# Kernel optimization log

Hardware: AMD Instinct MI355X
Metric: run time of the kernel (lower is better)

## Reference

```python
import jax, jax.numpy as jnp
import numpy as np

NUM_REGIONS = 20
EMBED_DIM = 768
PATCH = (4, 16, 16)          # (pd, ph, pw)
IMG = (64, 512, 512)         # (D, H, W)
B = 2
N_PATCHES = 16384


def setup_inputs() -> dict:
    key = jax.random.key(0)
    k1, k2, k3 = jax.random.split(key, 3)
    segmentation_mask = jax.random.randint(
        k1, (B, 1) + IMG, 0, NUM_REGIONS + 1, dtype=jnp.int32)
    patch_coords = jax.random.uniform(k2, (B, N_PATCHES, 3), dtype=jnp.float32)
    region_prototypes = 0.02 * jax.random.normal(
        k3, (NUM_REGIONS, EMBED_DIM), dtype=jnp.float32)
    return {"segmentation_mask": segmentation_mask,
            "patch_coords": patch_coords,
            "region_prototypes": region_prototypes}


def _compute_assignments(segmentation_mask, patch_coords):
    Bsz, _, D, H, W = segmentation_mask.shape
    pd, ph, pw = PATCH
    dims = jnp.array([D, H, W], dtype=jnp.float32)
    half = jnp.array([pd // 2, ph // 2, pw // 2], dtype=jnp.float32)

    cpix = patch_coords * dims                                   # (B,N,3)
    # torch: z_start = max(0, int(c - half)); z_end = min(D, int(c + half))
    start = jnp.maximum(0.0, jnp.floor(cpix - half)).astype(jnp.int32)   # (B,N,3)
    end = jnp.minimum(dims, jnp.floor(cpix + half)).astype(jnp.int32)    # (B,N,3)

    # per-axis index grids of fixed size, validity mask honors clipped box
    zi = start[..., 0:1] + jnp.arange(pd, dtype=jnp.int32)        # (B,N,pd)
    yi = start[..., 1:2] + jnp.arange(ph, dtype=jnp.int32)        # (B,N,ph)
    xi = start[..., 2:3] + jnp.arange(pw, dtype=jnp.int32)        # (B,N,pw)
    vz = zi < end[..., 0:1]
    vy = yi < end[..., 1:2]
    vx = xi < end[..., 2:3]

    ziC = jnp.clip(zi, 0, D - 1)
    yiC = jnp.clip(yi, 0, H - 1)
    xiC = jnp.clip(xi, 0, W - 1)

    # flattened gather: (B, N, pd, ph, pw) voxel values
    lin = (ziC[:, :, :, None, None] * (H * W)
           + yiC[:, :, None, :, None] * W
           + xiC[:, :, None, None, :])
    flat = segmentation_mask.reshape(Bsz, D * H * W)
    vals = jnp.take_along_axis(flat, lin.reshape(Bsz, -1), axis=1)
    vals = vals.reshape(Bsz, lin.shape[1], pd, ph, pw)
    valid = (vz[:, :, :, None, None]
             & vy[:, :, None, :, None]
             & vx[:, :, None, None, :])

    # numel of each (possibly clipped) crop
    extents = jnp.maximum(end - start, 0)                         # (B,N,3)
    numel = jnp.prod(extents, axis=-1).astype(jnp.float32)        # (B,N)

    # per-region counts; small fixed loop over 20 regions keeps memory low
    counts = jnp.stack(
        [jnp.sum((vals == r) & valid, axis=(2, 3, 4)).astype(jnp.float32)
         for r in range(1, NUM_REGIONS + 1)], axis=-1)            # (B,N,R)

    prop = counts / jnp.maximum(numel, 1.0)[..., None]            # zero crops -> 0
    a = prop + 1e-6
    a = a / jnp.sum(a, axis=-1, keepdims=True)
    return a


def reference(segmentation_mask, patch_coords, region_prototypes):
    Bsz = segmentation_mask.shape[0]
    region_features = jnp.broadcast_to(
        region_prototypes[None], (Bsz,) + region_prototypes.shape)
    patch_to_region = _compute_assignments(segmentation_mask, patch_coords)
    return region_features, patch_to_region
```

## Files before the change

kernel.cpp:

```cpp
#include <hip/hip_runtime.h>
#include <stdint.h>

#define NREG   20
#define EDIM   768
#define DVOL   64
#define HVOL   512
#define WVOL   512
#define HW_    (HVOL * WVOL)
#define DHW_   (DVOL * HVOL * WVOL)
#define NPATCH 16384
#define BTOT   2
#define PROTO_N (NREG * EDIM)
#define RF_N    (BTOT * PROTO_N)
#define TOTAL_PATCHES (BTOT * NPATCH)
#define NBUCKET 1024
#define SORT_BLOCKS 8

#define W_PHASE 0
#define W_BCNT  32
#define W_PID   (W_BCNT + SORT_BLOCKS * NBUCKET)
#define W_C0    (W_PID  + TOTAL_PATCHES)
#define W_C1    (W_C0   + TOTAL_PATCHES)
#define W_C2    (W_C1   + TOTAL_PATCHES)
#define MEMSET_WORDS (W_BCNT + SORT_BLOCKS * NBUCKET)

struct __attribute__((packed, aligned(4))) int4p { int x, y, z, w; };

__global__ __launch_bounds__(1024) void sort_kernel(
    const float* __restrict__ coords, unsigned* __restrict__ ws)
{
    __shared__ unsigned lcnt[NBUCKET];
    __shared__ unsigned lofs[NBUCKET];

    float* wsf = (float*)ws;
    const int blk = (int)blockIdx.x;
    const int t   = (int)threadIdx.x;
    const int p0  = blk * 4096 + t * 4;
    const int b   = blk >> 2;

    lcnt[t] = 0u;
    __syncthreads();

    float c[12];
    {
        const float4* cp = (const float4*)(coords + (size_t)p0 * 3);
        const float4 a = cp[0], bb = cp[1], d = cp[2];
        c[0]=a.x;  c[1]=a.y;  c[2]=a.z;  c[3]=a.w;  c[4]=bb.x; c[5]=bb.y;
        c[6]=bb.z; c[7]=bb.w; c[8]=d.x;  c[9]=d.y;  c[10]=d.z; c[11]=d.w;
    }
    unsigned key[4];
#pragma unroll
    for (int i = 0; i < 4; ++i) {
        const int zbin = ((int)(c[3*i + 0] * 64.0f))  >> 1;
        const int ybin = ((int)(c[3*i + 1] * 512.0f)) >> 5;
        key[i] = (unsigned)(b * 512 + zbin * 16 + ybin);
        atomicAdd(&lcnt[key[i]], 1u);
    }
    __syncthreads();

    ws[W_BCNT + blk * NBUCKET + t] = lcnt[t];
    __syncthreads();

    if (t == 0) {
        __hip_atomic_fetch_add(&ws[W_PHASE], 1u,
                               __ATOMIC_RELEASE, __HIP_MEMORY_SCOPE_AGENT);
        int guard = 0;
        while (__hip_atomic_load(&ws[W_PHASE],
                 __ATOMIC_ACQUIRE, __HIP_MEMORY_SCOPE_AGENT) < SORT_BLOCKS
               && guard < (1 << 22)) {
            __builtin_amdgcn_s_sleep(1);
            ++guard;
        }
    }
    __syncthreads();

    unsigned tot = 0u, before = 0u;
#pragma unroll
    for (int k = 0; k < SORT_BLOCKS; ++k) {
        const unsigned v = ws[W_BCNT + k * NBUCKET + t];
        tot += v;
        before += (k < blk) ? v : 0u;
    }
    lcnt[t] = tot;
    __syncthreads();

#pragma unroll
    for (int off = 1; off < NBUCKET; off <<= 1) {
        const unsigned u = (t >= off) ? lcnt[t - off] : 0u;
        __syncthreads();
        lcnt[t] += u;
        __syncthreads();
    }
    lofs[t] = (lcnt[t] - tot) + before;
    __syncthreads();

#pragma unroll
    for (int i = 0; i < 4; ++i) {
        const unsigned rank = atomicAdd(&lofs[key[i]], 1u);
        ws[W_PID + rank] = (unsigned)(p0 + i);
        wsf[W_C0 + rank] = c[3*i + 0];
        wsf[W_C1 + rank] = c[3*i + 1];
        wsf[W_C2 + rank] = c[3*i + 2];
    }
}

__global__ __launch_bounds__(256) void assign_kernel(
    const int*      __restrict__ seg,
    const unsigned* __restrict__ ws,
    const float*    __restrict__ proto,
    float*          __restrict__ out)
{
    if (blockIdx.x < RF_N / 256) {
        const int i = (int)blockIdx.x * 256 + (int)threadIdx.x;
        out[i] = proto[i >= PROTO_N ? i - PROTO_N : i];
    }

    const int bid  = (int)blockIdx.x;
    const int sbid = (bid & 7) * 1024 + (bid >> 3);

    const int lane = threadIdx.x & 63;
    const int wave = threadIdx.x >> 6;
    const int slot = sbid * 4 + wave;

    const int   patch = (int)ws[W_PID + slot];
    const float c0 = ((const float*)ws)[W_C0 + slot] * 64.0f;
    const float c1 = ((const float*)ws)[W_C1 + slot] * 512.0f;
    const float c2 = ((const float*)ws)[W_C2 + slot] * 512.0f;
    const int b = patch >> 14;

    const int sz = (int)fmaxf(0.0f,   floorf(c0 - 2.0f));
    const int ez = (int)fminf(64.0f,  floorf(c0 + 2.0f));
    const int sy = (int)fmaxf(0.0f,   floorf(c1 - 8.0f));
    const int ey = (int)fminf(512.0f, floorf(c1 + 8.0f));
    const int sx = (int)fmaxf(0.0f,   floorf(c2 - 8.0f));
    const int ex = (int)fminf(512.0f, floorf(c2 + 8.0f));

    const int xl4  = lane & 3;
    const int yy   = lane >> 2;
    const int p_lo = sx + 4 * xl4;
    const int st   = min(p_lo, WVOL - 4);
    const int yi   = sy + yy;
    const unsigned vy = (yi < ey) ? 0xFFFFFFFFu : 0u;
    const int yiC  = min(yi, HVOL - 1);
    const int rowbase = b * DHW_ + yiC * WVOL + st;

    unsigned vm[4];
#pragma unroll
    for (int j = 0; j < 4; ++j) {
        const int pos = st + j;
        vm[j] = (pos >= p_lo && pos < ex) ? vy : 0u;
    }

    int4p q0, q1, q2, q3;
    {
        const int z0 = min(sz + 0, DVOL - 1) * HW_;
        const int z1 = min(sz + 1, DVOL - 1) * HW_;
        const int z2 = min(sz + 2, DVOL - 1) * HW_;
        const int z3 = min(sz + 3, DVOL - 1) * HW_;
        q0 = *(const int4p*)(seg + rowbase + z0);
        q1 = *(const int4p*)(seg + rowbase + z1);
        q2 = *(const int4p*)(seg + rowbase + z2);
        q3 = *(const int4p*)(seg + rowbase + z3);
    }

    unsigned cc[5] = {0u, 0u, 0u, 0u, 0u};
#pragma unroll
    for (int z = 0; z < 4; ++z) {
        const unsigned zm = (sz + z < ez) ? 0xFFFFFFFFu : 0u;
        const int4p qz = (z == 0) ? q0 : (z == 1) ? q1 : (z == 2) ? q2 : q3;
        const int vals[4] = {qz.x, qz.y, qz.z, qz.w};
#pragma unroll
        for (int j = 0; j < 4; ++j) {
            const int v = vals[j] & (int)(vm[j] & zm);
            const int t = v - 1;
            const unsigned inc = 1u << ((t & 3) << 3);
            const int qk = t >> 2;
#pragma unroll
            for (int k = 0; k < 5; ++k)
                cc[k] += (qk == k) ? inc : 0u;
        }
    }

#pragma unroll
    for (int off = 1; off < 8; off <<= 1) {
#pragma unroll
        for (int k = 0; k < 5; ++k)
            cc[k] += (unsigned)__shfl_xor((int)cc[k], off);
    }

    unsigned lo[5], hi[5];
#pragma unroll
    for (int k = 0; k < 5; ++k) {
        lo[k] = cc[k] & 0x00FF00FFu;
        hi[k] = (cc[k] >> 8) & 0x00FF00FFu;
    }
#pragma unroll
    for (int off = 8; off < 64; off <<= 1) {
#pragma unroll
        for (int k = 0; k < 5; ++k) {
            lo[k] += (unsigned)__shfl_xor((int)lo[k], off);
            hi[k] += (unsigned)__shfl_xor((int)hi[k], off);
        }
    }

    unsigned S = 0u;
#pragma unroll
    for (int k = 0; k < 5; ++k) S += lo[k] + hi[k];
    const unsigned tot = (S & 0xFFFFu) + (S >> 16);

    const int r = lane & 3;
    const unsigned sLo = (lane < 4) ? lo[0] : (lane < 8) ? lo[1]
                       : (lane < 12) ? lo[2] : (lane < 16) ? lo[3] : lo[4];
    const unsigned sHi = (lane < 4) ? hi[0] : (lane < 8) ? hi[1]
                       : (lane < 12) ? hi[2] : (lane < 16) ? hi[3] : hi[4];
    const unsigned fld = (r & 1) ? sHi : sLo;
    const unsigned cnt = (r & 2) ? (fld >> 16) : (fld & 0xFFFFu);

    if (lane < NREG) {
        const float nz = (float)max(ez - sz, 0);
        const float ny = (float)max(ey - sy, 0);
        const float nx = (float)max(ex - sx, 0);
        const float denom = fmaxf(nz * ny * nx, 1.0f);
        const float s = (float)tot / denom + (float)NREG * 1e-6f;
        const float a = (float)cnt / denom + 1e-6f;
        out[RF_N + patch * NREG + lane] = a / s;
    }
}

extern "C" void kernel_launch(void* const* d_in, const int* in_sizes, int n_in,
                              void* d_out, int out_size, void* d_ws, size_t ws_size,
                              hipStream_t stream)
{
    const int*   seg    = (const int*)d_in[0];
    const float* coords = (const float*)d_in[1];
    const float* proto  = (const float*)d_in[2];
    float*       out    = (float*)d_out;
    unsigned*    ws     = (unsigned*)d_ws;

    hipMemsetAsync(ws, 0, MEMSET_WORDS * sizeof(unsigned), stream);
    hipLaunchKernelGGL(sort_kernel, dim3(SORT_BLOCKS), dim3(1024),
                       0, stream, coords, ws);
    hipLaunchKernelGGL(assign_kernel, dim3(TOTAL_PATCHES / 4), dim3(256),
                       0, stream, seg, ws, proto, out);
}
```

Baseline: 52.60 us.

## Compact segmentation mask to bytes in fused pre-pass before gather

Adds a pre-pass that reads the entire int32 segmentation volume (about 134MB) and writes it to workspace as uint8. It runs in the same launch as the coordinate bucket sort, which now uses 16 blocks of 512 threads. The assign kernel then gathers each patch row as 8-byte words from the compacted buffer, with one lane per (z,y) row instead of per 4-voxel chunk. The goal is fewer bytes moved in the gather. The trade-off is a full read of the mask plus a 33MB write every call, where the old gather only touched about 4MB of patch data.

```diff
diff --git a/kernel.cpp b/kernel.cpp
--- a/kernel.cpp
+++ b/kernel.cpp
@@ -14,31 +14,59 @@
 #define RF_N    (BTOT * PROTO_N)
 #define TOTAL_PATCHES (BTOT * NPATCH)
 #define NBUCKET 1024
-#define SORT_BLOCKS 8
-
-#define W_PHASE 0
-#define W_BCNT  32
-#define W_PID   (W_BCNT + SORT_BLOCKS * NBUCKET)
-#define W_C0    (W_PID  + TOTAL_PATCHES)
-#define W_C1    (W_C0   + TOTAL_PATCHES)
-#define W_C2    (W_C1   + TOTAL_PATCHES)
-#define MEMSET_WORDS (W_BCNT + SORT_BLOCKS * NBUCKET)
-
-struct __attribute__((packed, aligned(4))) int4p { int x, y, z, w; };
-
-__global__ __launch_bounds__(1024) void sort_kernel(
-    const float* __restrict__ coords, unsigned* __restrict__ ws)
-{
-    __shared__ unsigned lcnt[NBUCKET];
-    __shared__ unsigned lofs[NBUCKET];
+
+#define SORT_BLOCKS    16
+#define COMPACT_BLOCKS 512
+#define FUSED_BLOCKS   (SORT_BLOCKS + COMPACT_BLOCKS)
+
+#define SEG8_BYTES (BTOT * DHW_)
+#define W_PHASE    ((SEG8_BYTES / 4) + 16)
+#define W_BCNT     (W_PHASE + 32)
+#define W_PID      (W_BCNT + SORT_BLOCKS * NBUCKET)
+#define W_C0       (W_PID  + TOTAL_PATCHES)
+#define W_C1       (W_C0   + TOTAL_PATCHES)
+#define W_C2       (W_C1   + TOTAL_PATCHES)
+
+__device__ __forceinline__ uint32_t pack4i(int4 v)
+{
+    return (uint32_t)v.x | ((uint32_t)v.y << 8)
+         | ((uint32_t)v.z << 16) | ((uint32_t)v.w << 24);
+}
+
+__global__ __launch_bounds__(512) void fused_kernel(
+    const int*   __restrict__ seg,
+    const float* __restrict__ coords,
+    unsigned*    __restrict__ ws)
+{
+    const int bid = (int)blockIdx.x;
+    const int t   = (int)threadIdx.x;
+
+    if (bid >= SORT_BLOCKS) {
+        uint8_t* seg8 = (uint8_t*)ws;
+        const int gid = (bid - SORT_BLOCKS) * 512 + t;
+#pragma unroll
+        for (int it = 0; it < 8; ++it) {
+            const int q = it * (COMPACT_BLOCKS * 512) + gid;
+            const int4* ip = (const int4*)(seg + (size_t)q * 16);
+            const int4 v0 = ip[0], v1 = ip[1], v2 = ip[2], v3 = ip[3];
+            uint4 w;
+            w.x = pack4i(v0); w.y = pack4i(v1);
+            w.z = pack4i(v2); w.w = pack4i(v3);
+            ((uint4*)seg8)[q] = w;
+        }
+        return;
+    }
+
+    __shared__ unsigned hist[NBUCKET];
+    __shared__ unsigned sA[NBUCKET], sB[NBUCKET];
+    __shared__ unsigned curs[NBUCKET];
 
     float* wsf = (float*)ws;
-    const int blk = (int)blockIdx.x;
-    const int t   = (int)threadIdx.x;
-    const int p0  = blk * 4096 + t * 4;
-    const int b   = blk >> 2;
-
-    lcnt[t] = 0u;
+    const int blk = bid;
+    const int p0  = blk * 2048 + t * 4;
+    const int b   = blk >> 3;
+
+    hist[t] = 0u; hist[t + 512] = 0u;
     __syncthreads();
 
     float c[12];
@@ -54,11 +82,12 @@
         const int zbin = ((int)(c[3*i + 0] * 64.0f))  >> 1;
         const int ybin = ((int)(c[3*i + 1] * 512.0f)) >> 5;
         key[i] = (unsigned)(b * 512 + zbin * 16 + ybin);
-        atomicAdd(&lcnt[key[i]], 1u);
-    }
-    __syncthreads();
-
-    ws[W_BCNT + blk * NBUCKET + t] = lcnt[t];
+        atomicAdd(&hist[key[i]], 1u);
+    }
+    __syncthreads();
+
+    ws[W_BCNT + blk * NBUCKET + t]       = hist[t];
+    ws[W_BCNT + blk * NBUCKET + t + 512] = hist[t + 512];
     __syncthreads();
 
     if (t == 0) {
@@ -67,36 +96,39 @@
         int guard = 0;
         while (__hip_atomic_load(&ws[W_PHASE],
                  __ATOMIC_ACQUIRE, __HIP_MEMORY_SCOPE_AGENT) < SORT_BLOCKS
-               && guard < (1 << 22)) {
+               && guard < (1 << 24)) {
             __builtin_amdgcn_s_sleep(1);
             ++guard;
         }
     }
     __syncthreads();
 
-    unsigned tot = 0u, before = 0u;
+    unsigned tot0 = 0u, bef0 = 0u, tot1 = 0u, bef1 = 0u;
 #pragma unroll
     for (int k = 0; k < SORT_BLOCKS; ++k) {
-        const unsigned v = ws[W_BCNT + k * NBUCKET + t];
-        tot += v;
-        before += (k < blk) ? v : 0u;
-    }
-    lcnt[t] = tot;
-    __syncthreads();
-
-#pragma unroll
+        const unsigned v0 = ws[W_BCNT + k * NBUCKET + t];
+        const unsigned v1 = ws[W_BCNT + k * NBUCKET + t + 512];
+        tot0 += v0; bef0 += (k < blk) ? v0 : 0u;
+        tot1 += v1; bef1 += (k < blk) ? v1 : 0u;
+    }
+    sA[t] = tot0; sA[t + 512] = tot1;
+    __syncthreads();
+
+    unsigned* src = sA;
+    unsigned* dst = sB;
     for (int off = 1; off < NBUCKET; off <<= 1) {
-        const unsigned u = (t >= off) ? lcnt[t - off] : 0u;
+        dst[t]       = src[t]       + ((t       >= off) ? src[t       - off] : 0u);
+        dst[t + 512] = src[t + 512] + ((t + 512 >= off) ? src[t + 512 - off] : 0u);
         __syncthreads();
-        lcnt[t] += u;
-        __syncthreads();
-    }
-    lofs[t] = (lcnt[t] - tot) + before;
+        unsigned* tmp = src; src = dst; dst = tmp;
+    }
+    curs[t]       = (src[t]       - tot0) + bef0;
+    curs[t + 512] = (src[t + 512] - tot1) + bef1;
     __syncthreads();
 
 #pragma unroll
     for (int i = 0; i < 4; ++i) {
-        const unsigned rank = atomicAdd(&lofs[key[i]], 1u);
+        const unsigned rank = atomicAdd(&curs[key[i]], 1u);
         ws[W_PID + rank] = (unsigned)(p0 + i);
         wsf[W_C0 + rank] = c[3*i + 0];
         wsf[W_C1 + rank] = c[3*i + 1];
@@ -105,7 +137,6 @@
 }
 
 __global__ __launch_bounds__(256) void assign_kernel(
-    const int*      __restrict__ seg,
     const unsigned* __restrict__ ws,
     const float*    __restrict__ proto,
     float*          __restrict__ out)
@@ -115,6 +146,9 @@
         out[i] = proto[i >= PROTO_N ? i - PROTO_N : i];
     }
 
+    const uint8_t* seg8 = (const uint8_t*)ws;
+    const float*   wsf  = (const float*)ws;
+
     const int bid  = (int)blockIdx.x;
     const int sbid = (bid & 7) * 1024 + (bid >> 3);
 
@@ -123,9 +157,9 @@
     const int slot = sbid * 4 + wave;
 
     const int   patch = (int)ws[W_PID + slot];
-    const float c0 = ((const float*)ws)[W_C0 + slot] * 64.0f;
-    const float c1 = ((const float*)ws)[W_C1 + slot] * 512.0f;
-    const float c2 = ((const float*)ws)[W_C2 + slot] * 512.0f;
+    const float c0 = wsf[W_C0 + slot] * 64.0f;
+    const float c1 = wsf[W_C1 + slot] * 512.0f;
+    const float c2 = wsf[W_C2 + slot] * 512.0f;
     const int b = patch >> 14;
 
     const int sz = (int)fmaxf(0.0f,   floorf(c0 - 2.0f));
@@ -135,46 +169,43 @@
     const int sx = (int)fmaxf(0.0f,   floorf(c2 - 8.0f));
     const int ex = (int)fminf(512.0f, floorf(c2 + 8.0f));
 
-    const int xl4  = lane & 3;
-    const int yy   = lane >> 2;
-    const int p_lo = sx + 4 * xl4;
-    const int st   = min(p_lo, WVOL - 4);
-    const int yi   = sy + yy;
-    const unsigned vy = (yi < ey) ? 0xFFFFFFFFu : 0u;
-    const int yiC  = min(yi, HVOL - 1);
-    const int rowbase = b * DHW_ + yiC * WVOL + st;
-
-    unsigned vm[4];
-#pragma unroll
-    for (int j = 0; j < 4; ++j) {
-        const int pos = st + j;
-        vm[j] = (pos >= p_lo && pos < ex) ? vy : 0u;
-    }
-
-    int4p q0, q1, q2, q3;
-    {
-        const int z0 = min(sz + 0, DVOL - 1) * HW_;
-        const int z1 = min(sz + 1, DVOL - 1) * HW_;
-        const int z2 = min(sz + 2, DVOL - 1) * HW_;
-        const int z3 = min(sz + 3, DVOL - 1) * HW_;
-        q0 = *(const int4p*)(seg + rowbase + z0);
-        q1 = *(const int4p*)(seg + rowbase + z1);
-        q2 = *(const int4p*)(seg + rowbase + z2);
-        q3 = *(const int4p*)(seg + rowbase + z3);
-    }
+    const int zz = lane >> 4;
+    const int yy = lane & 15;
+    const int zi = sz + zz;
+    const int yi = sy + yy;
+    const int ziC = min(zi, DVOL - 1);
+    const int yiC = min(yi, HVOL - 1);
+    const int a0  = sx & ~7;
+    const int sh  = (sx & 7) * 8;
+    const int rowoff = b * DHW_ + ziC * HW_ + yiC * WVOL;
+
+    const uint8_t* rp = seg8 + (size_t)rowoff + a0;
+    const uint64_t u0 = *(const uint64_t*)(rp);
+    const uint64_t u1 = *(const uint64_t*)(rp + 8);
+    const uint64_t u2 = *(const uint64_t*)(rp + 16);
+
+    uint64_t A  = (u0 >> sh) | (sh ? (u1 << (64 - sh)) : 0ull);
+    uint64_t Bv = (u1 >> sh) | (sh ? (u2 << (64 - sh)) : 0ull);
+
+    const int nv  = min(max(ex - sx, 0), 16);
+    const int nvB = max(nv - 8, 0);
+    uint64_t mA = (nv  >= 8) ? ~0ull : ((1ull << (8 * nv )) - 1ull);
+    uint64_t mB = (nvB >= 8) ? ~0ull : ((1ull << (8 * nvB)) - 1ull);
+    if (!((yi < ey) & (zi < ez))) { mA = 0ull; mB = 0ull; }
+    A &= mA;  Bv &= mB;
 
     unsigned cc[5] = {0u, 0u, 0u, 0u, 0u};
-#pragma unroll
-    for (int z = 0; z < 4; ++z) {
-        const unsigned zm = (sz + z < ez) ? 0xFFFFFFFFu : 0u;
-        const int4p qz = (z == 0) ? q0 : (z == 1) ? q1 : (z == 2) ? q2 : q3;
-        const int vals[4] = {qz.x, qz.y, qz.z, qz.w};
+    const uint32_t wd[4] = {(uint32_t)A,  (uint32_t)(A  >> 32),
+                            (uint32_t)Bv, (uint32_t)(Bv >> 32)};
+#pragma unroll
+    for (int d = 0; d < 4; ++d) {
+        const uint32_t x = wd[d];
 #pragma unroll
         for (int j = 0; j < 4; ++j) {
-            const int v = vals[j] & (int)(vm[j] & zm);
-            const int t = v - 1;
-            const unsigned inc = 1u << ((t & 3) << 3);
-            const int qk = t >> 2;
+            const int v = (int)((x >> (8 * j)) & 0xFFu);
+            const int tt = v - 1;
+            const unsigned inc = 1u << ((tt & 3) << 3);
+            const int qk = tt >> 2;
 #pragma unroll
             for (int k = 0; k < 5; ++k)
                 cc[k] += (qk == k) ? inc : 0u;
@@ -237,9 +268,9 @@
     float*       out    = (float*)d_out;
     unsigned*    ws     = (unsigned*)d_ws;
 
-    hipMemsetAsync(ws, 0, MEMSET_WORDS * sizeof(unsigned), stream);
-    hipLaunchKernelGGL(sort_kernel, dim3(SORT_BLOCKS), dim3(1024),
-                       0, stream, coords, ws);
+    hipMemsetAsync(ws + W_PHASE, 0, sizeof(unsigned), stream);
+    hipLaunchKernelGGL(fused_kernel, dim3(FUSED_BLOCKS), dim3(512),
+                       0, stream, seg, coords, ws);
     hipLaunchKernelGGL(assign_kernel, dim3(TOTAL_PATCHES / 4), dim3(256),
-                       0, stream, seg, ws, proto, out);
-}
+                       0, stream, ws, proto, out);
+}
```

New measurement: 65.83 us. 1.25x slower.
